# Performance work log

Hardware: AMD Instinct MI355X
Metric: run time of the kernel (lower is better)

Reference implementation:

```python
import jax, jax.numpy as jnp
import numpy as np

_MASK = -1.0e9
_EPS = 1e-8
B, N, E, D, L, NREL, TAU = 4, 2048, 32768, 128, 3, 1000, 0.1


def setup_inputs() -> dict:
    key = jax.random.key(0)
    ks = jax.random.split(key, 24)
    s = 0.05
    inp = {
        'edge_index': jax.random.randint(ks[0], (B, 2, E), 0, N, dtype=jnp.int32),
        'rels': jax.random.randint(ks[1], (B, E), 0, NREL, dtype=jnp.int32),
        'scores': jax.random.uniform(ks[2], (B, E), dtype=jnp.float32),
        'edge_conf_mask': jax.random.randint(ks[3], (B, E), 0, 2) > 0,
        'edge_mask': jax.random.randint(ks[4], (B, E), 0, 2) > 0,
        'mask': jnp.ones((B, N), dtype=bool),
        'r_query_embed': jax.random.normal(ks[5], (B, D), dtype=jnp.float32),
        'conf_embeds': jax.random.normal(ks[6], (B, E, D), dtype=jnp.float32),
        'rel_table': jax.random.normal(ks[7], (NREL, D), dtype=jnp.float32) * s,
        'beta_W': jax.random.normal(ks[8], (D, 1), dtype=jnp.float32) * s,
        'beta_b': jnp.zeros((1,), dtype=jnp.float32),
        'msg_W': jax.random.normal(ks[9], (L, 5 * D, D), dtype=jnp.float32) * s,
        'msg_b': jnp.zeros((L, D), dtype=jnp.float32),
        'upd_W': jax.random.normal(ks[10], (L, D, D), dtype=jnp.float32) * s,
        'upd_b': jnp.zeros((L, D), dtype=jnp.float32),
        'ln_g': jnp.ones((D,), dtype=jnp.float32),
        'ln_b': jnp.zeros((D,), dtype=jnp.float32),
        'att_W': jax.random.normal(ks[11], (L, 3 * D, 1), dtype=jnp.float32) * s,
        'att_b': jnp.zeros((L, 1), dtype=jnp.float32),
        'den_W1': jax.random.normal(ks[12], (3 * D, D), dtype=jnp.float32) * s,
        'den_b1': jnp.zeros((D,), dtype=jnp.float32),
        'den_W2': jax.random.normal(ks[13], (D, 1), dtype=jnp.float32) * s,
        'den_b2': jnp.zeros((1,), dtype=jnp.float32),
    }
    return inp


def _layer_norm(x, g, b, eps=1e-5):
    mu = jnp.mean(x, axis=-1, keepdims=True)
    var = jnp.var(x, axis=-1, keepdims=True)
    return (x - mu) * jax.lax.rsqrt(var + eps) * g + b


def reference(edge_index, rels, scores, edge_conf_mask, edge_mask, mask,
              r_query_embed, conf_embeds, rel_table, beta_W, beta_b,
              msg_W, msg_b, upd_W, upd_b, ln_g, ln_b, att_W, att_b,
              den_W1, den_b1, den_W2, den_b2):
    Bb, Nn = mask.shape
    Ee = edge_index.shape[2]
    d = rel_table.shape[1]
    bidx = jnp.arange(Bb)[:, None]                      # [B,1] batch index for scatter/gather
    src = edge_index[:, 0, :]                           # [B,E]
    tgt = edge_index[:, 1, :]                           # [B,E]

    h_init = jnp.zeros((Bb, Nn, d), dtype=rel_table.dtype).at[:, 0, :].set(1.0)
    h = h_init
    h_r = rel_table[rels]                               # [B,E,D]
    rq = jnp.broadcast_to(r_query_embed[:, None, :], (Bb, Ee, d))
    em = edge_mask.astype(h.dtype)[..., None]           # [B,E,1]

    # edge denoiser gate
    gate_in = jnp.concatenate([h_r, rq, conf_embeds], axis=-1)
    den = jax.nn.sigmoid(jax.nn.relu(gate_in @ den_W1 + den_b1) @ den_W2 + den_b2) * em

    beta = jax.nn.sigmoid((h_r + rq) @ beta_W + beta_b)             # [B,E,1]
    gate_known = jax.nn.sigmoid((scores[..., None] - beta) / TAU)
    gate = jnp.where(edge_conf_mask[..., None], gate_known, 0.5)

    outs = []
    for k in range(msg_W.shape[0]):
        h_src = h[bidx, src]                            # [B,E,D] gather
        h_init_src = h_init[bidx, src]
        msg_in = jnp.concatenate([h_src * h_r, h_src, h_init_src, h_r, conf_embeds], axis=-1)
        raw_msg = jax.nn.relu(msg_in @ msg_W[k] + msg_b[k])         # [B,E,D]

        att_in = jnp.concatenate([raw_msg, h_r, rq], axis=-1)
        att = jax.nn.leaky_relu((att_in @ att_W[k] + att_b[k])[..., 0], 0.01)
        att = jnp.where(edge_mask, att, _MASK)

        # scatter-softmax over edges sharing a target node
        mx = jnp.full((Bb, Nn), _MASK, dtype=att.dtype).at[bidx, tgt].max(att)
        ex = jnp.exp(att - mx[bidx, tgt])
        sm = jnp.zeros((Bb, Nn), dtype=att.dtype).at[bidx, tgt].add(ex)
        alpha = ex / (sm[bidx, tgt] + _EPS)             # [B,E]

        wmsg = gate * alpha[..., None] * raw_msg * em * den
        aggr = jnp.zeros_like(h).at[bidx, tgt].add(wmsg)
        h = _layer_norm(h + aggr @ upd_W[k] + upd_b[k], ln_g, ln_b)
        outs.append(h[:, 0, :])
    return jnp.stack(outs, axis=1)                      # [B,L,D]
```

## Files before the change

### kernel.cpp

```cpp
#include <hip/hip_runtime.h>
#include <stdint.h>
#include <math.h>

#define BB 4
#define NNODE 2048
#define NE 32768
#define DDIM 128
#define NL 3
#define NRELS 1000
#define MASKV -1000000000.0f

typedef unsigned short ushort_t;
typedef __attribute__((ext_vector_type(8))) short bfrag;
typedef __attribute__((ext_vector_type(4))) float f4;

__device__ __forceinline__ float sigf(float x){ return 1.0f/(1.0f+expf(-x)); }

__device__ __forceinline__ float bf2f(ushort_t u){
  union { unsigned int i; float f; } v; v.i = ((unsigned int)u) << 16; return v.f;
}
__device__ __forceinline__ ushort_t f2bf(float x){
  union { float f; unsigned int u; } v; v.f = x;
  unsigned int r = (v.u + 0x7FFFu + ((v.u >> 16) & 1u)) >> 16;
  return (ushort_t)r;
}
__device__ __forceinline__ float bflo(unsigned u){
  union{unsigned i;float f;}v; v.i=u<<16; return v.f;
}
__device__ __forceinline__ float bfhi(unsigned u){
  union{unsigned i;float f;}v; v.i=u&0xFFFF0000u; return v.f;
}
__device__ __forceinline__ unsigned pmul_bf(unsigned a, unsigned b){
  return (unsigned)f2bf(bflo(a)*bflo(b)) | ((unsigned)f2bf(bfhi(a)*bfhi(b))<<16);
}
__device__ __forceinline__ unsigned packbf(float a, float b){
  return (unsigned)f2bf(a) | ((unsigned)f2bf(b)<<16);
}

__global__ void probe_mask_kernel(const void* cm_raw, int* flag){
  int t = threadIdx.x;
  const int* ip = (const int*)cm_raw;
  unsigned v = (unsigned)ip[t];
  bool i32ok = (v <= 1u);
  bool f32ok = (v == 0u) || (v == 0x3F800000u);
  unsigned long long bi = __ballot(i32ok);
  unsigned long long bf_ = __ballot(f32ok);
  if (t == 0){
    int f;
    if (bi == ~0ULL) f = 0;
    else if (bf_ == ~0ULL) f = 1;
    else f = 2;
    *flag = f;
  }
}

__global__ void prep_kernel(const void* cm_raw, const void* em_raw, const int* __restrict__ flag,
    uint8_t* __restrict__ cm, uint8_t* __restrict__ em, int* __restrict__ deg,
    const float* __restrict__ relt, ushort_t* __restrict__ relt_bf,
    const float* __restrict__ rq, ushort_t* __restrict__ rq_bf,
    int* __restrict__ src_c, int* __restrict__ rel_c, int* __restrict__ ge_c,
    float* __restrict__ h, ushort_t* __restrict__ h_bf)
{
  int gid = blockIdx.x*256 + threadIdx.x;
  if (gid < BB*NE){
    int f = *flag; uint8_t c, e;
    if (f == 0){ c = ((const int*)cm_raw)[gid]!=0;   e = ((const int*)em_raw)[gid]!=0; }
    else if (f == 1){ c = ((const float*)cm_raw)[gid]!=0.0f; e = ((const float*)em_raw)[gid]!=0.0f; }
    else { c = ((const uint8_t*)cm_raw)[gid]!=0; e = ((const uint8_t*)em_raw)[gid]!=0; }
    cm[gid]=c; em[gid]=e;
    src_c[gid]=0; rel_c[gid]=0; ge_c[gid]=0;
  }
  if (gid < BB*NNODE) deg[gid]=0;
  if (gid < NRELS*DDIM/4){
    float4 v = *(const float4*)&relt[gid*4];
    ushort4 o; o.x=f2bf(v.x); o.y=f2bf(v.y); o.z=f2bf(v.z); o.w=f2bf(v.w);
    *(ushort4*)&relt_bf[gid*4] = o;
  }
  if (gid < BB*DDIM/4){
    float4 v = *(const float4*)&rq[gid*4];
    ushort4 o; o.x=f2bf(v.x); o.y=f2bf(v.y); o.z=f2bf(v.z); o.w=f2bf(v.w);
    *(ushort4*)&rq_bf[gid*4] = o;
  }
  {
    int base = gid*4;
    int nd = base & (NNODE*DDIM - 1);
    bool one = (nd < DDIM);
    float4 hv = one ? (float4){1.f,1.f,1.f,1.f} : (float4){0.f,0.f,0.f,0.f};
    ushort4 hb = one ? (ushort4){0x3F80,0x3F80,0x3F80,0x3F80} : (ushort4){0,0,0,0};
    *(float4*)&h[base] = hv;
    *(ushort4*)&h_bf[base] = hb;
  }
}

__global__ void csr_hist_kernel(const int* __restrict__ edge_index,
                                const uint8_t* __restrict__ em, int* __restrict__ deg){
  int gid = blockIdx.x*256 + threadIdx.x;
  if (!em[gid]) return;
  int b = gid >> 15, e = gid & (NE-1);
  int tgt = edge_index[(b<<16) + NE + e];
  atomicAdd(&deg[(b<<11) + tgt], 1);
}
__global__ void csr_scan_kernel(const int* __restrict__ deg,
                                int* __restrict__ base, int* __restrict__ cursor){
  __shared__ int part[256];
  int t = threadIdx.x;
  int loc[32]; int s = 0;
  #pragma unroll
  for (int i=0;i<32;++i){ loc[i] = deg[t*32+i]; s += loc[i]; }
  part[t] = s; __syncthreads();
  for (int off=1; off<256; off<<=1){
    int v = (t >= off) ? part[t-off] : 0;
    __syncthreads();
    part[t] += v;
    __syncthreads();
  }
  int ex = (t==0) ? 0 : part[t-1];
  #pragma unroll
  for (int i=0;i<32;++i){ base[t*32+i] = ex; cursor[t*32+i] = ex; ex += loc[i]; }
  if (t == 255) base[256*32] = ex;
}
__global__ void csr_scatter_kernel(const int* __restrict__ edge_index,
                                   const int* __restrict__ rels,
                                   const uint8_t* __restrict__ em,
                                   int* __restrict__ cursor,
                                   int* __restrict__ src_c, int* __restrict__ rel_c,
                                   int* __restrict__ ge_c){
  int gid = blockIdx.x*256 + threadIdx.x;
  if (!em[gid]) return;
  int b = gid >> 15, e = gid & (NE-1);
  int tgt = edge_index[(b<<16) + NE + e];
  int src = edge_index[(b<<16) + e];
  int pos = atomicAdd(&cursor[(b<<11) + tgt], 1);
  src_c[pos] = (b<<11) | src;
  rel_c[pos] = rels[gid];
  ge_c[pos]  = gid;
}

__global__ void precomp_tables_kernel(
    const float* __restrict__ relt, const float* __restrict__ rq,
    const float* __restrict__ attW, const float* __restrict__ betaW,
    float* __restrict__ att_rel, float* __restrict__ att_rq,
    float* __restrict__ beta_rel, float* __restrict__ beta_rq)
{
  int wid = (blockIdx.x*256 + threadIdx.x) >> 6;
  int lane = threadIdx.x & 63;
  if (wid >= 3*NRELS + 3*BB + NRELS + BB) return;
  const float* vec; const float* w; float* dst; int di;
  if (wid < 3*NRELS){
    int k = wid/NRELS, rl = wid%NRELS;
    vec = relt + rl*DDIM; w = attW + k*384 + 128; dst = att_rel; di = wid;
  } else if (wid < 3*NRELS + 3*BB){
    int idx = wid - 3*NRELS; int k = idx/BB, b = idx%BB;
    vec = rq + b*DDIM; w = attW + k*384 + 256; dst = att_rq; di = idx;
  } else if (wid < 3*NRELS + 3*BB + NRELS){
    int rl = wid - (3*NRELS + 3*BB);
    vec = relt + rl*DDIM; w = betaW; dst = beta_rel; di = rl;
  } else {
    int b = wid - (3*NRELS + 3*BB + NRELS);
    vec = rq + b*DDIM; w = betaW; dst = beta_rq; di = b;
  }
  float s = vec[lane]*w[lane] + vec[lane+64]*w[lane+64];
  #pragma unroll
  for (int off=32; off; off>>=1) s += __shfl_xor(s, off, 64);
  if (lane == 0) dst[di] = s;
}

__global__ void vtables_kernel(const float* __restrict__ relt, const float* __restrict__ rq,
    const float* __restrict__ msgW, const float* __restrict__ msgb,
    const float* __restrict__ denW1, const float* __restrict__ denb1,
    float* __restrict__ relmsg, float* __restrict__ relhh0,
    float* __restrict__ denrel, float* __restrict__ denrq,
    float* __restrict__ initvec, float* __restrict__ src0vec)
{
  int wv = (blockIdx.x*256 + threadIdx.x) >> 6;
  int lane = threadIdx.x & 63;
  if (wv >= 5008) return;
  const float* A = nullptr; const float* W; int K = 128; float* out; const float* bias = nullptr;
  if (wv < 3000){ int k=wv/1000, rl=wv%1000;
    A=relt+rl*128; W=msgW+(size_t)k*81920+49152; out=relmsg+(size_t)wv*128; bias=msgb+k*128; }
  else if (wv < 4000){ int rl=wv-3000;
    A=relt+rl*128; W=msgW; out=relhh0+(size_t)rl*128; }
  else if (wv < 5000){ int rl=wv-4000;
    A=relt+rl*128; W=denW1; out=denrel+(size_t)rl*128; }
  else if (wv < 5004){ int b=wv-5000;
    A=rq+b*128; W=denW1+16384; out=denrq+b*128; bias=denb1; }
  else if (wv < 5007){ int k=wv-5004;
    W=msgW+(size_t)k*81920+32768; out=initvec+k*128; }
  else { W=msgW+16384; K=256; out=src0vec; }
  float a0=0.f, a1=0.f;
  for (int kk=0; kk<K; ++kk){
    float av = A ? A[kk] : 1.0f;
    a0 = fmaf(av, W[kk*128+lane],    a0);
    a1 = fmaf(av, W[kk*128+lane+64], a1);
  }
  if (bias){ a0 += bias[lane]; a1 += bias[lane+64]; }
  out[lane]=a0; out[lane+64]=a1;
}

__global__ void build_wimg_kernel(const float* __restrict__ msgW,
                                  const float* __restrict__ denW1,
                                  ushort_t* __restrict__ img_msg,
                                  ushort_t* __restrict__ img_den){
  int e = blockIdx.x*256 + threadIdx.x;
  if (e >= 14*8192) return;
  int img_id = e >> 13;
  int ei = e & 8191;
  int j = ei >> 6;
  int kk = (((ei & 63) << 1) ^ ((j & 7) << 4)) >> 1;
  if (img_id < 12){
    int k = img_id >> 2, c = img_id & 3;
    int rowbase = (c < 2) ? c*64 : 512 + (c-2)*64;
    img_msg[(size_t)img_id*8192 + ei] = f2bf(msgW[(size_t)k*81920 + (rowbase+kk)*128 + j]);
  } else {
    int c = img_id - 12;
    int rowbase = 256 + c*64;
    img_den[(size_t)c*8192 + ei] = f2bf(denW1[(size_t)(rowbase+kk)*128 + j]);
  }
}

__global__ __launch_bounds__(256,2) void coef_mfma_kernel(
    const int* __restrict__ nact_p,
    const int* __restrict__ rel_c, const int* __restrict__ ge_c,
    const float* __restrict__ conf, const ushort_t* __restrict__ img_den,
    const float* __restrict__ denrel, const float* __restrict__ denrq,
    const float* __restrict__ denW2, const float* __restrict__ denb2,
    const float* __restrict__ scores, const uint8_t* __restrict__ cm,
    const float* __restrict__ beta_rel, const float* __restrict__ beta_rq,
    const float* __restrict__ betab,
    float* __restrict__ coef_c)
{
  __shared__ char lds[32768];
  __shared__ int rel_s[128], ge_s[128];
  __shared__ float w2_s[128];

  const int blk = blockIdx.x;
  const int ci0 = blk << 7;
  const int nact = *nact_p;
  if (ci0 >= nact) return;
  const int t = threadIdx.x;
  if (t < 128){ rel_s[t]=rel_c[ci0+t]; ge_s[t]=ge_c[ci0+t]; w2_s[t]=denW2[t]; }

  const int lane=t&63, wid=t>>6;
  const int wr=wid>>1, wc=wid&1;
  const int rbase=wr<<6, cbase=wc<<6;
  const int lr=lane&15, lk=lane>>4;
  const int swz=(lane&7)<<4;
  const int g=t&7, row0=t>>3;
  const int aswz=(g<<4)^((row0&7)<<4);

  f4 acc[4][4];
  #pragma unroll
  for (int m=0;m<4;++m)
    #pragma unroll
    for (int n=0;n<4;++n) acc[m][n]=(f4){0.f,0.f,0.f,0.f};

  const uint4* imgp = (const uint4*)img_den;
  float4 pf0[4], pf1[4];
  uint4 pb[4];
  __syncthreads();

  auto issueA = [&](int ch){
    const int d0=(ch&1)<<6;
    #pragma unroll
    for (int i=0;i<4;++i){
      int row=row0+(i<<5);
      const float* cp = conf + (((size_t)ge_s[row])<<7) + d0 + (g<<3);
      pf0[i]=*(const float4*)cp; pf1[i]=*(const float4*)(cp+4);
    }
    #pragma unroll
    for (int i=0;i<4;++i) pb[i]=imgp[ch*1024+(i<<8)+t];
  };

  issueA(0);
  #pragma unroll
  for (int ch=0; ch<2; ++ch){
    #pragma unroll
    for (int i=0;i<4;++i){
      int row=row0+(i<<5);
      uint4 val;
      val.x=packbf(pf0[i].x,pf0[i].y); val.y=packbf(pf0[i].z,pf0[i].w);
      val.z=packbf(pf1[i].x,pf1[i].y); val.w=packbf(pf1[i].z,pf1[i].w);
      *(uint4*)(lds + row*128 + aswz) = val;
    }
    *(uint4*)(lds+16384+(t<<4))        = pb[0];
    *(uint4*)(lds+16384+(t<<4)+4096)   = pb[1];
    *(uint4*)(lds+16384+(t<<4)+8192)   = pb[2];
    *(uint4*)(lds+16384+(t<<4)+12288)  = pb[3];
    __syncthreads();
    if (ch < 1) issueA(ch+1);
    #pragma unroll
    for (int s=0;s<2;++s){
      bfrag af[4], bfr[4];
      #pragma unroll
      for (int m=0;m<4;++m)
        af[m] = *(const bfrag*)(lds + (rbase+(m<<4)+lr)*128 + (((s<<6)+(lk<<4)) ^ swz));
      #pragma unroll
      for (int n=0;n<4;++n)
        bfr[n] = *(const bfrag*)(lds + 16384 + (cbase+(n<<4)+lr)*128 + (((s<<6)+(lk<<4)) ^ swz));
      #pragma unroll
      for (int m=0;m<4;++m)
        #pragma unroll
        for (int n=0;n<4;++n)
          acc[m][n] = __builtin_amdgcn_mfma_f32_16x16x32_bf16(af[m], bfr[n], acc[m][n], 0,0,0);
    }
    __syncthreads();
  }

  #pragma unroll
  for (int m=0;m<4;++m)
    #pragma unroll
    for (int n=0;n<4;++n)
      #pragma unroll
      for (int q=0;q<4;++q){
        int row=rbase+(m<<4)+(lk<<2)+q;
        int col=cbase+(n<<4)+lr;
        *(ushort_t*)(lds+(row<<8)+((col<<1)^((row&7)<<4))) = f2bf(acc[m][n][q]);
      }
  __syncthreads();

  #pragma unroll
  for (int i=0;i<8;++i){
    int u=t+(i<<8), row=u>>4, gg=u&15, c0=gg<<3;
    uint4 v = *(const uint4*)(lds+(row<<8)+((gg<<4)^((row&7)<<4)));
    float vv[8] = {bflo(v.x),bfhi(v.x),bflo(v.y),bfhi(v.y),
                   bflo(v.z),bfhi(v.z),bflo(v.w),bfhi(v.w)};
    int rel=rel_s[row], ge=ge_s[row], b=ge>>15;
    const float* dr = denrel + ((size_t)rel<<7) + c0;
    const float* dq = denrq + (b<<7) + c0;
    float part=0.f;
    #pragma unroll
    for (int j=0;j<8;++j){
      float m = fmaxf(vv[j] + dr[j] + dq[j], 0.f);
      part = fmaf(m, w2_s[c0+j], part);
    }
    #pragma unroll
    for (int off=1; off<16; off<<=1) part += __shfl_xor(part, off, 16);
    if (gg == 0){
      float den = sigf(part + denb2[0]);
      float beta = sigf(beta_rel[rel] + beta_rq[b] + betab[0]);
      float gt = cm[ge] ? sigf((scores[ge]-beta)*10.0f) : 0.5f;
      coef_c[ci0+row] = gt * den;
    }
  }
}

template<bool L0>
__global__ __launch_bounds__(256,2) void msg_mfma_kernel(
    const int* __restrict__ nact_p,
    const int* __restrict__ src_c, const int* __restrict__ rel_c,
    const int* __restrict__ ge_c,
    const ushort_t* __restrict__ relt_bf, const float* __restrict__ conf,
    const ushort_t* __restrict__ h_bf, const float* __restrict__ H1,
    const ushort_t* __restrict__ img_msg,
    const float* __restrict__ relmsg, const float* __restrict__ relhh0,
    const float* __restrict__ src0vec, const float* __restrict__ initvec,
    const float* __restrict__ attW, const float* __restrict__ attb,
    const float* __restrict__ att_rel, const float* __restrict__ att_rq,
    ushort_t* __restrict__ raw_c, float* __restrict__ att_c, int layer)
{
  constexpr int NCH = L0 ? 2 : 4;
  __shared__ char lds[32768];
  __shared__ int src_s[128], rel_s[128], ge_s[128];
  __shared__ float attw_s[128];

  const int blk = blockIdx.x;
  const int ci0 = blk << 7;
  const int nact = *nact_p;
  if (ci0 >= nact) return;
  const int t = threadIdx.x;
  if (t < 128){
    src_s[t]=src_c[ci0+t]; rel_s[t]=rel_c[ci0+t]; ge_s[t]=ge_c[ci0+t];
    attw_s[t]=attW[layer*384+t];
  }

  const int lane=t&63, wid=t>>6;
  const int wr=wid>>1, wc=wid&1;
  const int rbase=wr<<6, cbase=wc<<6;
  const int lr=lane&15, lk=lane>>4;
  const int swz=(lane&7)<<4;
  const int g=t&7, row0=t>>3;
  const int aswz=(g<<4)^((row0&7)<<4);

  f4 acc[4][4];
  #pragma unroll
  for (int m=0;m<4;++m)
    #pragma unroll
    for (int n=0;n<4;++n) acc[m][n]=(f4){0.f,0.f,0.f,0.f};

  const uint4* imgp = (const uint4*)(img_msg + (size_t)layer*4*8192);
  uint4 pa[4], pr[4], pb[4];
  float4 pf0[4], pf1[4];
  __syncthreads();

  auto issueA = [&](int ch){
    const int d0=(ch&1)<<6;
    const bool cf = L0 || (ch>=2);
    #pragma unroll
    for (int i=0;i<4;++i){
      int row=row0+(i<<5);
      if (cf){
        const float* cp = conf + (((size_t)ge_s[row])<<7) + d0 + (g<<3);
        pf0[i]=*(const float4*)cp; pf1[i]=*(const float4*)(cp+4);
      } else {
        pa[i]=*(const uint4*)&h_bf[(((size_t)src_s[row])<<7)+d0+(g<<3)];
        pr[i]=*(const uint4*)&relt_bf[(((size_t)rel_s[row])<<7)+d0+(g<<3)];
      }
    }
    int ic = L0 ? ch+2 : ch;
    #pragma unroll
    for (int i=0;i<4;++i) pb[i]=imgp[ic*1024+(i<<8)+t];
  };

  issueA(0);
  #pragma unroll
  for (int ch=0; ch<NCH; ++ch){
    const bool cf = L0 || (ch>=2);
    #pragma unroll
    for (int i=0;i<4;++i){
      int row=row0+(i<<5);
      uint4 val;
      if (cf){
        val.x=packbf(pf0[i].x,pf0[i].y); val.y=packbf(pf0[i].z,pf0[i].w);
        val.z=packbf(pf1[i].x,pf1[i].y); val.w=packbf(pf1[i].z,pf1[i].w);
      } else {
        val.x=pmul_bf(pa[i].x,pr[i].x); val.y=pmul_bf(pa[i].y,pr[i].y);
        val.z=pmul_bf(pa[i].z,pr[i].z); val.w=pmul_bf(pa[i].w,pr[i].w);
      }
      *(uint4*)(lds + row*128 + aswz) = val;
    }
    *(uint4*)(lds+16384+(t<<4))        = pb[0];
    *(uint4*)(lds+16384+(t<<4)+4096)   = pb[1];
    *(uint4*)(lds+16384+(t<<4)+8192)   = pb[2];
    *(uint4*)(lds+16384+(t<<4)+12288)  = pb[3];
    __syncthreads();
    if (ch < NCH-1) issueA(ch+1);
    #pragma unroll
    for (int s=0;s<2;++s){
      bfrag af[4], bfr[4];
      #pragma unroll
      for (int m=0;m<4;++m)
        af[m] = *(const bfrag*)(lds + (rbase+(m<<4)+lr)*128 + (((s<<6)+(lk<<4)) ^ swz));
      #pragma unroll
      for (int n=0;n<4;++n)
        bfr[n] = *(const bfrag*)(lds + 16384 + (cbase+(n<<4)+lr)*128 + (((s<<6)+(lk<<4)) ^ swz));
      #pragma unroll
      for (int m=0;m<4;++m)
        #pragma unroll
        for (int n=0;n<4;++n)
          acc[m][n] = __builtin_amdgcn_mfma_f32_16x16x32_bf16(af[m], bfr[n], acc[m][n], 0,0,0);
    }
    __syncthreads();
  }

  #pragma unroll
  for (int m=0;m<4;++m)
    #pragma unroll
    for (int n=0;n<4;++n)
      #pragma unroll
      for (int q=0;q<4;++q){
        int row=rbase+(m<<4)+(lk<<2)+q;
        int col=cbase+(n<<4)+lr;
        *(ushort_t*)(lds+(row<<8)+((col<<1)^((row&7)<<4))) = f2bf(acc[m][n][q]);
      }
  __syncthreads();

  #pragma unroll
  for (int i=0;i<8;++i){
    int u=t+(i<<8), row=u>>4, gg=u&15, c0=gg<<3;
    uint4 v = *(const uint4*)(lds+(row<<8)+((gg<<4)^((row&7)<<4)));
    float vv[8] = {bflo(v.x),bfhi(v.x),bflo(v.y),bfhi(v.y),
                   bflo(v.z),bfhi(v.z),bflo(v.w),bfhi(v.w)};
    int rel=rel_s[row], sc=src_s[row], ge=ge_s[row], b=ge>>15;
    const float* rm = relmsg + (((size_t)(layer*1000+rel))<<7) + c0;
    float bias[8];
    #pragma unroll
    for (int j=0;j<8;++j) bias[j] = rm[j];
    if (!L0){
      const float* hp = H1 + (((size_t)sc)<<7) + c0;
      #pragma unroll
      for (int j=0;j<8;++j) bias[j] += hp[j];
      if ((sc & (NNODE-1)) == 0){
        const float* iv = initvec + layer*128 + c0;
        #pragma unroll
        for (int j=0;j<8;++j) bias[j] += iv[j];
      }
    } else {
      if ((sc & (NNODE-1)) == 0){
        const float* rh = relhh0 + ((size_t)rel<<7) + c0;
        const float* sv = src0vec + c0;
        #pragma unroll
        for (int j=0;j<8;++j) bias[j] += rh[j] + sv[j];
      }
    }
    float part=0.f;
    unsigned o0,o1,o2,o3;
    {
      float m0=fmaxf(vv[0]+bias[0],0.f), m1=fmaxf(vv[1]+bias[1],0.f);
      float m2=fmaxf(vv[2]+bias[2],0.f), m3=fmaxf(vv[3]+bias[3],0.f);
      float m4=fmaxf(vv[4]+bias[4],0.f), m5=fmaxf(vv[5]+bias[5],0.f);
      float m6=fmaxf(vv[6]+bias[6],0.f), m7=fmaxf(vv[7]+bias[7],0.f);
      part = m0*attw_s[c0] + m1*attw_s[c0+1] + m2*attw_s[c0+2] + m3*attw_s[c0+3]
           + m4*attw_s[c0+4] + m5*attw_s[c0+5] + m6*attw_s[c0+6] + m7*attw_s[c0+7];
      o0=packbf(m0,m1); o1=packbf(m2,m3); o2=packbf(m4,m5); o3=packbf(m6,m7);
    }
    uint4 ov; ov.x=o0; ov.y=o1; ov.z=o2; ov.w=o3;
    *(uint4*)&raw_c[(((size_t)(ci0+row))<<7) + c0] = ov;
    #pragma unroll
    for (int off=1; off<16; off<<=1) part += __shfl_xor(part, off, 16);
    if (gg == 0){
      float a = part + att_rel[layer*NRELS+rel] + att_rq[layer*BB+b] + attb[layer];
      a = (a >= 0.f) ? a : 0.01f*a;
      att_c[ci0+row] = a;
    }
  }
}

#define FMA4(acc, a, bv) do { \
    acc.x = fmaf(a, bv.x, acc.x); \
    acc.y = fmaf(a, bv.y, acc.y); \
    acc.z = fmaf(a, bv.z, acc.z); \
    acc.w = fmaf(a, bv.w, acc.w); } while(0)

__global__ __launch_bounds__(256,2) void h1_gemm_kernel(
    const float* __restrict__ h, const float* __restrict__ msgW,
    float* __restrict__ H1, int layer)
{
  __shared__ float As[64*65];
  __shared__ float Bs[64*128];
  const int t = threadIdx.x, blk = blockIdx.x;
  const int n0 = blk << 6;
  const int c = t & 15, r = t >> 4;
  float4 acc0[4], acc1[4];
  #pragma unroll
  for (int i=0;i<4;++i){ acc0[i]=make_float4(0,0,0,0); acc1[i]=make_float4(0,0,0,0); }
  const float* wbase = msgW + (size_t)layer*81920 + 16384;

  for (int ch=0; ch<2; ++ch){
    __syncthreads();
    #pragma unroll
    for (int l=0;l<16;++l){
      int idx=(l<<8)+t, ei=idx>>6, kk=idx&63;
      As[ei*65+kk] = h[(size_t)(n0+ei)*DDIM + (ch<<6) + kk];
    }
    #pragma unroll
    for (int l=0;l<32;++l){
      int idx=(l<<8)+t, kk=idx>>7, j=idx&127;
      Bs[(kk<<7)+j] = wbase[((ch<<6)+kk)*DDIM + j];
    }
    __syncthreads();
    #pragma unroll 4
    for (int kk=0;kk<64;++kk){
      const float4 b0 = *(const float4*)&Bs[(kk<<7) + (c<<2)];
      const float4 b1 = *(const float4*)&Bs[(kk<<7) + 64 + (c<<2)];
      #pragma unroll
      for (int i=0;i<4;++i){
        const float a = As[((r<<2)+i)*65 + kk];
        FMA4(acc0[i], a, b0);
        FMA4(acc1[i], a, b1);
      }
    }
  }
  const int col0 = c << 2;
  #pragma unroll
  for (int i=0;i<4;++i){
    const int row = n0 + (r<<2) + i;
    *(float4*)&H1[(size_t)row*DDIM + col0]      = make_float4(acc0[i].x,acc0[i].y,acc0[i].z,acc0[i].w);
    *(float4*)&H1[(size_t)row*DDIM + 64 + col0] = make_float4(acc1[i].x,acc1[i].y,acc1[i].z,acc1[i].w);
  }
}

__global__ __launch_bounds__(128) void node_agg_kernel(
    const int* __restrict__ base,
    const float* __restrict__ att_c, const float* __restrict__ coef_c,
    const ushort_t* __restrict__ raw_c, float* __restrict__ aggr)
{
  const int n = blockIdx.x;
  const int t = threadIdx.x;
  const int b0 = base[n], b1 = base[n+1];
  const int deg = b1 - b0;
  if (deg == 0){ aggr[((size_t)n<<7)+t] = 0.f; return; }
  __shared__ float w_s[128];
  __shared__ float red[4];
  float mx = -3.0e38f;
  for (int j=t; j<deg; j+=128) mx = fmaxf(mx, att_c[b0+j]);
  #pragma unroll
  for (int o=1;o<64;o<<=1) mx = fmaxf(mx, __shfl_xor(mx, o, 64));
  if ((t&63)==0) red[t>>6] = mx;
  __syncthreads();
  mx = fmaxf(red[0], red[1]);
  float s = 0.f;
  for (int j=t; j<deg; j+=128) s += expf(att_c[b0+j]-mx);
  #pragma unroll
  for (int o=1;o<64;o<<=1) s += __shfl_xor(s, o, 64);
  if ((t&63)==0) red[2+(t>>6)] = s;
  __syncthreads();
  const float inv = 1.0f/((red[2]+red[3]) + 1e-8f);
  float accv = 0.f;
  for (int jb=0; jb<deg; jb+=128){
    int jj = jb + t;
    __syncthreads();
    if (jj < deg) w_s[t] = coef_c[b0+jj] * expf(att_c[b0+jj]-mx) * inv;
    __syncthreads();
    int lim = min(128, deg-jb);
    for (int j=0; j<lim; ++j)
      accv = fmaf(w_s[j], bf2f(raw_c[(((size_t)(b0+jb+j))<<7)+t]), accv);
  }
  aggr[((size_t)n<<7)+t] = accv;
}

__global__ __launch_bounds__(256,2) void update_kernel(
    const float* __restrict__ aggr, const float* __restrict__ updW,
    const float* __restrict__ updb,
    const float* __restrict__ lng, const float* __restrict__ lnb,
    float* __restrict__ h, ushort_t* __restrict__ h_bf,
    float* __restrict__ out, int layer)
{
  __shared__ float As[64*65];
  __shared__ float Bs[64*128];
  const int t = threadIdx.x, blk = blockIdx.x;
  const int n0 = blk << 6;
  const int c = t & 15, r = t >> 4;
  float4 acc0[4], acc1[4];
  #pragma unroll
  for (int i=0;i<4;++i){ acc0[i]=make_float4(0,0,0,0); acc1[i]=make_float4(0,0,0,0); }
  const float* wbase = updW + (size_t)layer*DDIM*DDIM;

  for (int ch=0; ch<2; ++ch){
    __syncthreads();
    #pragma unroll
    for (int l=0;l<16;++l){
      int idx=(l<<8)+t, ei=idx>>6, kk=idx&63;
      As[ei*65+kk] = aggr[(size_t)(n0+ei)*DDIM + (ch<<6) + kk];
    }
    #pragma unroll
    for (int l=0;l<32;++l){
      int idx=(l<<8)+t, kk=idx>>7, j=idx&127;
      Bs[(kk<<7)+j] = wbase[((ch<<6)+kk)*DDIM + j];
    }
    __syncthreads();
    #pragma unroll 4
    for (int kk=0;kk<64;++kk){
      const float4 b0 = *(const float4*)&Bs[(kk<<7) + (c<<2)];
      const float4 b1 = *(const float4*)&Bs[(kk<<7) + 64 + (c<<2)];
      #pragma unroll
      for (int i=0;i<4;++i){
        const float a = As[((r<<2)+i)*65 + kk];
        FMA4(acc0[i], a, b0);
        FMA4(acc1[i], a, b1);
      }
    }
  }

  const int col0 = c << 2;
  float ub0[4], ub1[4], g0[4], g1[4], lb0[4], lb1[4];
  #pragma unroll
  for (int q=0;q<4;++q){
    ub0[q] = updb[layer*DDIM + col0+q];  ub1[q] = updb[layer*DDIM + 64+col0+q];
    g0[q]  = lng[col0+q];                g1[q]  = lng[64+col0+q];
    lb0[q] = lnb[col0+q];                lb1[q] = lnb[64+col0+q];
  }

  #pragma unroll
  for (int i=0;i<4;++i){
    const int row = n0 + (r<<2) + i;
    float* hrow = h + (size_t)row*DDIM;
    float4 h0 = *(float4*)&hrow[col0];
    float4 h1 = *(float4*)&hrow[64+col0];
    float x0[4], x1[4];
    x0[0] = h0.x + acc0[i].x + ub0[0];
    x0[1] = h0.y + acc0[i].y + ub0[1];
    x0[2] = h0.z + acc0[i].z + ub0[2];
    x0[3] = h0.w + acc0[i].w + ub0[3];
    x1[0] = h1.x + acc1[i].x + ub1[0];
    x1[1] = h1.y + acc1[i].y + ub1[1];
    x1[2] = h1.z + acc1[i].z + ub1[2];
    x1[3] = h1.w + acc1[i].w + ub1[3];
    float s = 0.f, s2 = 0.f;
    #pragma unroll
    for (int q=0;q<4;++q){ s += x0[q]+x1[q]; s2 += x0[q]*x0[q] + x1[q]*x1[q]; }
    #pragma unroll
    for (int off=1; off<16; off<<=1){
      s  += __shfl_xor(s,  off, 16);
      s2 += __shfl_xor(s2, off, 16);
    }
    const float mu = s * (1.0f/128.0f);
    const float var = s2 * (1.0f/128.0f) - mu*mu;
    const float rstd = rsqrtf(var + 1e-5f);
    float4 y0, y1;
    y0.x = (x0[0]-mu)*rstd*g0[0] + lb0[0];
    y0.y = (x0[1]-mu)*rstd*g0[1] + lb0[1];
    y0.z = (x0[2]-mu)*rstd*g0[2] + lb0[2];
    y0.w = (x0[3]-mu)*rstd*g0[3] + lb0[3];
    y1.x = (x1[0]-mu)*rstd*g1[0] + lb1[0];
    y1.y = (x1[1]-mu)*rstd*g1[1] + lb1[1];
    y1.z = (x1[2]-mu)*rstd*g1[2] + lb1[2];
    y1.w = (x1[3]-mu)*rstd*g1[3] + lb1[3];
    *(float4*)&hrow[col0] = y0;
    *(float4*)&hrow[64+col0] = y1;
    ushort4 z0, z1;
    z0.x=f2bf(y0.x); z0.y=f2bf(y0.y); z0.z=f2bf(y0.z); z0.w=f2bf(y0.w);
    z1.x=f2bf(y1.x); z1.y=f2bf(y1.y); z1.z=f2bf(y1.z); z1.w=f2bf(y1.w);
    *(ushort4*)&h_bf[(size_t)row*DDIM + col0] = z0;
    *(ushort4*)&h_bf[(size_t)row*DDIM + 64 + col0] = z1;
    if ((row & (NNODE-1)) == 0){
      const int bb_ = row >> 11;
      float* op = out + (size_t)(bb_*NL + layer)*DDIM;
      *(float4*)&op[col0] = y0;
      *(float4*)&op[64+col0] = y1;
    }
  }
}

extern "C" void kernel_launch(void* const* d_in, const int* in_sizes, int n_in,
                              void* d_out, int out_size, void* d_ws, size_t ws_size,
                              hipStream_t stream) {
  const int*   edge_index = (const int*)d_in[0];
  const int*   rels       = (const int*)d_in[1];
  const float* scores     = (const float*)d_in[2];
  const void*  cm_raw     = d_in[3];
  const void*  em_raw     = d_in[4];
  const float* rq    = (const float*)d_in[6];
  const float* conf  = (const float*)d_in[7];
  const float* relt  = (const float*)d_in[8];
  const float* betaW = (const float*)d_in[9];
  const float* betab = (const float*)d_in[10];
  const float* msgW  = (const float*)d_in[11];
  const float* msgb  = (const float*)d_in[12];
  const float* updW  = (const float*)d_in[13];
  const float* updb  = (const float*)d_in[14];
  const float* lng   = (const float*)d_in[15];
  const float* lnb   = (const float*)d_in[16];
  const float* attW  = (const float*)d_in[17];
  const float* attb  = (const float*)d_in[18];
  const float* denW1 = (const float*)d_in[19];
  const float* denb1 = (const float*)d_in[20];
  const float* denW2 = (const float*)d_in[21];
  const float* denb2 = (const float*)d_in[22];
  float* out = (float*)d_out;
  char* ws = (char*)d_ws;

  size_t off = 0;
  float* h        = (float*)(ws + off); off += (size_t)BB*NNODE*DDIM*4;
  ushort_t* h_bf  = (ushort_t*)(ws + off); off += (size_t)BB*NNODE*DDIM*2;
  float* aggr     = (float*)(ws + off); off += (size_t)BB*NNODE*DDIM*4;
  float* H1       = (float*)(ws + off); off += (size_t)BB*NNODE*DDIM*4;
  ushort_t* raw_c = (ushort_t*)(ws + off); off += (size_t)BB*NE*DDIM*2;
  float* att_c    = (float*)(ws + off); off += (size_t)BB*NE*4;
  float* coef_c   = (float*)(ws + off); off += (size_t)BB*NE*4;
  int* src_c      = (int*)(ws + off); off += (size_t)BB*NE*4;
  int* rel_c      = (int*)(ws + off); off += (size_t)BB*NE*4;
  int* ge_c       = (int*)(ws + off); off += (size_t)BB*NE*4;
  int* deg        = (int*)(ws + off); off += (size_t)BB*NNODE*4;
  int* base       = (int*)(ws + off); off += (size_t)(BB*NNODE+16)*4;
  int* cursor     = (int*)(ws + off); off += (size_t)BB*NNODE*4;
  ushort_t* relt_bf = (ushort_t*)(ws + off); off += (size_t)NRELS*DDIM*2 + 64;
  ushort_t* rq_bf   = (ushort_t*)(ws + off); off += (size_t)BB*DDIM*2 + 64;
  ushort_t* img_msg = (ushort_t*)(ws + off); off += (size_t)12*8192*2;
  ushort_t* img_den = (ushort_t*)(ws + off); off += (size_t)2*8192*2;
  float* relmsg   = (float*)(ws + off); off += (size_t)3*NRELS*DDIM*4;
  float* relhh0   = (float*)(ws + off); off += (size_t)NRELS*DDIM*4;
  float* denrel   = (float*)(ws + off); off += (size_t)NRELS*DDIM*4;
  float* denrq    = (float*)(ws + off); off += (size_t)BB*DDIM*4;
  float* initvec  = (float*)(ws + off); off += 3*DDIM*4;
  float* src0vec  = (float*)(ws + off); off += DDIM*4;
  float* att_rel  = (float*)(ws + off); off += 3*NRELS*4 + 32;
  float* att_rq   = (float*)(ws + off); off += 64;
  float* beta_rel = (float*)(ws + off); off += NRELS*4 + 32;
  float* beta_rq  = (float*)(ws + off); off += 64;
  uint8_t* cm_dec = (uint8_t*)(ws + off); off += (size_t)BB*NE;
  uint8_t* em_dec = (uint8_t*)(ws + off); off += (size_t)BB*NE;
  int* flag       = (int*)(ws + off); off += 64;

  probe_mask_kernel<<<1, 64, 0, stream>>>(cm_raw, flag);
  prep_kernel<<<1024, 256, 0, stream>>>(cm_raw, em_raw, flag, cm_dec, em_dec, deg,
                                        relt, relt_bf, rq, rq_bf,
                                        src_c, rel_c, ge_c, h, h_bf);
  csr_hist_kernel<<<512, 256, 0, stream>>>(edge_index, em_dec, deg);
  csr_scan_kernel<<<1, 256, 0, stream>>>(deg, base, cursor);
  csr_scatter_kernel<<<512, 256, 0, stream>>>(edge_index, rels, em_dec, cursor,
                                              src_c, rel_c, ge_c);
  precomp_tables_kernel<<<1004, 256, 0, stream>>>(relt, rq, attW, betaW,
                                                  att_rel, att_rq, beta_rel, beta_rq);
  vtables_kernel<<<1252, 256, 0, stream>>>(relt, rq, msgW, msgb, denW1, denb1,
                                           relmsg, relhh0, denrel, denrq,
                                           initvec, src0vec);
  build_wimg_kernel<<<448, 256, 0, stream>>>(msgW, denW1, img_msg, img_den);
  coef_mfma_kernel<<<1024, 256, 0, stream>>>(base + BB*NNODE, rel_c, ge_c, conf, img_den,
                                             denrel, denrq, denW2, denb2,
                                             scores, cm_dec, beta_rel, beta_rq, betab,
                                             coef_c);
  for (int k = 0; k < NL; ++k){
    if (k == 0){
      msg_mfma_kernel<true><<<1024, 256, 0, stream>>>(base + BB*NNODE, src_c, rel_c, ge_c,
          relt_bf, conf, h_bf, H1, img_msg, relmsg, relhh0, src0vec, initvec,
          attW, attb, att_rel, att_rq, raw_c, att_c, k);
    } else {
      h1_gemm_kernel<<<128, 256, 0, stream>>>(h, msgW, H1, k);
      msg_mfma_kernel<false><<<1024, 256, 0, stream>>>(base + BB*NNODE, src_c, rel_c, ge_c,
          relt_bf, conf, h_bf, H1, img_msg, relmsg, relhh0, src0vec, initvec,
          attW, attb, att_rel, att_rq, raw_c, att_c, k);
    }
    node_agg_kernel<<<BB*NNODE, 128, 0, stream>>>(base, att_c, coef_c, raw_c, aggr);
    update_kernel<<<128, 256, 0, stream>>>(aggr, updW, updb, lng, lnb, h, h_bf, out, k);
  }
}
```

Baseline: 413.3 us.

## Compute relation tables with bf16 MFMA GEMM and fold small kernels together

The scalar vtables kernel is replaced. It used one wave per output row with serial FMA loops over 5000 relation-table rows. In its place, a bf16 MFMA tile GEMM (table_gemm_kernel) runs over swizzled bf16 weight images that build_wimg_kernel now also produces. The few remaining small vector products move into precomp_tables_kernel with an unrolled loop. The mask-format probe is folded into prep_kernel through a per-block ballot in shared memory. Together these cut two launches and the slow scalar table build, at the cost of bf16 rounding in tables that were fp32 before.

```diff
diff --git a/kernel.cpp b/kernel.cpp
--- a/kernel.cpp
+++ b/kernel.cpp
@@ -37,33 +37,27 @@
   return (unsigned)f2bf(a) | ((unsigned)f2bf(b)<<16);
 }
 
-__global__ void probe_mask_kernel(const void* cm_raw, int* flag){
-  int t = threadIdx.x;
-  const int* ip = (const int*)cm_raw;
-  unsigned v = (unsigned)ip[t];
-  bool i32ok = (v <= 1u);
-  bool f32ok = (v == 0u) || (v == 0x3F800000u);
-  unsigned long long bi = __ballot(i32ok);
-  unsigned long long bf_ = __ballot(f32ok);
-  if (t == 0){
-    int f;
-    if (bi == ~0ULL) f = 0;
-    else if (bf_ == ~0ULL) f = 1;
-    else f = 2;
-    *flag = f;
-  }
-}
-
-__global__ void prep_kernel(const void* cm_raw, const void* em_raw, const int* __restrict__ flag,
+__global__ void prep_kernel(const void* cm_raw, const void* em_raw,
     uint8_t* __restrict__ cm, uint8_t* __restrict__ em, int* __restrict__ deg,
     const float* __restrict__ relt, ushort_t* __restrict__ relt_bf,
     const float* __restrict__ rq, ushort_t* __restrict__ rq_bf,
     int* __restrict__ src_c, int* __restrict__ rel_c, int* __restrict__ ge_c,
     float* __restrict__ h, ushort_t* __restrict__ h_bf)
 {
+  __shared__ int flag_s;
+  if (threadIdx.x < 64){
+    unsigned v = ((const unsigned*)cm_raw)[threadIdx.x];
+    bool i32ok = (v <= 1u);
+    bool f32ok = (v == 0u) || (v == 0x3F800000u);
+    unsigned long long bi = __ballot(i32ok);
+    unsigned long long bf_ = __ballot(f32ok);
+    if (threadIdx.x == 0) flag_s = (bi==~0ULL) ? 0 : ((bf_==~0ULL) ? 1 : 2);
+  }
+  __syncthreads();
+  const int f = flag_s;
   int gid = blockIdx.x*256 + threadIdx.x;
   if (gid < BB*NE){
-    int f = *flag; uint8_t c, e;
+    uint8_t c, e;
     if (f == 0){ c = ((const int*)cm_raw)[gid]!=0;   e = ((const int*)em_raw)[gid]!=0; }
     else if (f == 1){ c = ((const float*)cm_raw)[gid]!=0.0f; e = ((const float*)em_raw)[gid]!=0.0f; }
     else { c = ((const uint8_t*)cm_raw)[gid]!=0; e = ((const uint8_t*)em_raw)[gid]!=0; }
@@ -139,15 +133,42 @@
 __global__ void precomp_tables_kernel(
     const float* __restrict__ relt, const float* __restrict__ rq,
     const float* __restrict__ attW, const float* __restrict__ betaW,
+    const float* __restrict__ msgW, const float* __restrict__ denW1,
+    const float* __restrict__ denb1,
     float* __restrict__ att_rel, float* __restrict__ att_rq,
-    float* __restrict__ beta_rel, float* __restrict__ beta_rq)
+    float* __restrict__ beta_rel, float* __restrict__ beta_rq,
+    float* __restrict__ denrq, float* __restrict__ initvec,
+    float* __restrict__ src0vec)
 {
   int wid = (blockIdx.x*256 + threadIdx.x) >> 6;
   int lane = threadIdx.x & 63;
-  if (wid >= 3*NRELS + 3*BB + NRELS + BB) return;
+  if (wid >= 4024) return;
+  if (wid >= 4016){
+    int widx = wid - 4016;
+    const float* A = nullptr; const float* W; int K = 128;
+    float* outp; const float* bias = nullptr;
+    if (widx < 4){ A = rq + widx*128; W = denW1 + 16384; outp = denrq + widx*128; bias = denb1; }
+    else if (widx < 7){ int k=widx-4; W = msgW + (size_t)k*81920 + 32768; outp = initvec + k*128; }
+    else { W = msgW + 16384; K = 256; outp = src0vec; }
+    float a0=0.f, a1=0.f;
+    for (int kk=0; kk<K; kk+=8){
+      float av[8], w0[8], w1[8];
+      #pragma unroll
+      for (int u=0;u<8;++u){
+        av[u] = A ? A[kk+u] : 1.0f;
+        w0[u] = W[(size_t)(kk+u)*128 + lane];
+        w1[u] = W[(size_t)(kk+u)*128 + lane + 64];
+      }
+      #pragma unroll
+      for (int u=0;u<8;++u){ a0 = fmaf(av[u], w0[u], a0); a1 = fmaf(av[u], w1[u], a1); }
+    }
+    if (bias){ a0 += bias[lane]; a1 += bias[lane+64]; }
+    outp[lane] = a0; outp[lane+64] = a1;
+    return;
+  }
   const float* vec; const float* w; float* dst; int di;
   if (wid < 3*NRELS){
-    int k = wid/NRELS, rl = wid%NRELS;
+    int k = wid/1000, rl = wid%1000;
     vec = relt + rl*DDIM; w = attW + k*384 + 128; dst = att_rel; di = wid;
   } else if (wid < 3*NRELS + 3*BB){
     int idx = wid - 3*NRELS; int k = idx/BB, b = idx%BB;
@@ -165,57 +186,130 @@
   if (lane == 0) dst[di] = s;
 }
 
-__global__ void vtables_kernel(const float* __restrict__ relt, const float* __restrict__ rq,
-    const float* __restrict__ msgW, const float* __restrict__ msgb,
-    const float* __restrict__ denW1, const float* __restrict__ denb1,
-    float* __restrict__ relmsg, float* __restrict__ relhh0,
-    float* __restrict__ denrel, float* __restrict__ denrq,
-    float* __restrict__ initvec, float* __restrict__ src0vec)
-{
-  int wv = (blockIdx.x*256 + threadIdx.x) >> 6;
-  int lane = threadIdx.x & 63;
-  if (wv >= 5008) return;
-  const float* A = nullptr; const float* W; int K = 128; float* out; const float* bias = nullptr;
-  if (wv < 3000){ int k=wv/1000, rl=wv%1000;
-    A=relt+rl*128; W=msgW+(size_t)k*81920+49152; out=relmsg+(size_t)wv*128; bias=msgb+k*128; }
-  else if (wv < 4000){ int rl=wv-3000;
-    A=relt+rl*128; W=msgW; out=relhh0+(size_t)rl*128; }
-  else if (wv < 5000){ int rl=wv-4000;
-    A=relt+rl*128; W=denW1; out=denrel+(size_t)rl*128; }
-  else if (wv < 5004){ int b=wv-5000;
-    A=rq+b*128; W=denW1+16384; out=denrq+b*128; bias=denb1; }
-  else if (wv < 5007){ int k=wv-5004;
-    W=msgW+(size_t)k*81920+32768; out=initvec+k*128; }
-  else { W=msgW+16384; K=256; out=src0vec; }
-  float a0=0.f, a1=0.f;
-  for (int kk=0; kk<K; ++kk){
-    float av = A ? A[kk] : 1.0f;
-    a0 = fmaf(av, W[kk*128+lane],    a0);
-    a1 = fmaf(av, W[kk*128+lane+64], a1);
-  }
-  if (bias){ a0 += bias[lane]; a1 += bias[lane+64]; }
-  out[lane]=a0; out[lane+64]=a1;
-}
-
 __global__ void build_wimg_kernel(const float* __restrict__ msgW,
                                   const float* __restrict__ denW1,
                                   ushort_t* __restrict__ img_msg,
-                                  ushort_t* __restrict__ img_den){
+                                  ushort_t* __restrict__ img_den,
+                                  ushort_t* __restrict__ img_tab){
   int e = blockIdx.x*256 + threadIdx.x;
-  if (e >= 14*8192) return;
+  if (e >= 22*8192) return;
   int img_id = e >> 13;
   int ei = e & 8191;
   int j = ei >> 6;
   int kk = (((ei & 63) << 1) ^ ((j & 7) << 4)) >> 1;
+  float v;
+  ushort_t* dst;
   if (img_id < 12){
     int k = img_id >> 2, c = img_id & 3;
     int rowbase = (c < 2) ? c*64 : 512 + (c-2)*64;
-    img_msg[(size_t)img_id*8192 + ei] = f2bf(msgW[(size_t)k*81920 + (rowbase+kk)*128 + j]);
+    v = msgW[(size_t)k*81920 + (rowbase+kk)*128 + j];
+    dst = img_msg + (size_t)img_id*8192;
+  } else if (img_id < 14){
+    int c = img_id - 12;
+    v = denW1[(size_t)(256 + c*64 + kk)*128 + j];
+    dst = img_den + (size_t)c*8192;
+  } else if (img_id < 20){
+    int idx = img_id - 14, k = idx >> 1, c = idx & 1;
+    v = msgW[(size_t)k*81920 + (384 + c*64 + kk)*128 + j];
+    dst = img_tab + (size_t)idx*8192;
   } else {
-    int c = img_id - 12;
-    int rowbase = 256 + c*64;
-    img_den[(size_t)c*8192 + ei] = f2bf(denW1[(size_t)(rowbase+kk)*128 + j]);
-  }
+    int c = img_id - 20;
+    v = denW1[(size_t)(c*64 + kk)*128 + j];
+    dst = img_tab + (size_t)(6+c)*8192;
+  }
+  dst[ei] = f2bf(v);
+}
+
+__global__ __launch_bounds__(256,2) void table_gemm_kernel(
+    const ushort_t* __restrict__ relt_bf, const ushort_t* __restrict__ img_msg,
+    const ushort_t* __restrict__ img_tab, const float* __restrict__ msgb,
+    float* __restrict__ relmsg, float* __restrict__ relhh0,
+    float* __restrict__ denrel)
+{
+  __shared__ char lds[32768];
+  __shared__ float bias_s[128];
+  const int blk = blockIdx.x;
+  const int job = blk % 5;
+  const int ri0 = (blk/5) << 7;
+  const int t = threadIdx.x;
+  const uint4* imgb;
+  float* outp;
+  if (job < 3){ imgb = (const uint4*)(img_tab + (size_t)(2*job)*8192); outp = relmsg + (size_t)job*NRELS*DDIM; }
+  else if (job == 3){ imgb = (const uint4*)img_msg; outp = relhh0; }
+  else { imgb = (const uint4*)(img_tab + (size_t)6*8192); outp = denrel; }
+  if (t < 128) bias_s[t] = (job < 3) ? msgb[job*128 + t] : 0.f;
+
+  const int lane=t&63, wid=t>>6;
+  const int wr=wid>>1, wc=wid&1;
+  const int rbase=wr<<6, cbase=wc<<6;
+  const int lr=lane&15, lk=lane>>4;
+  const int swz=(lane&7)<<4;
+  const int g=t&7, row0=t>>3;
+  const int aswz=(g<<4)^((row0&7)<<4);
+
+  f4 acc[4][4];
+  #pragma unroll
+  for (int m=0;m<4;++m)
+    #pragma unroll
+    for (int n=0;n<4;++n) acc[m][n]=(f4){0.f,0.f,0.f,0.f};
+
+  uint4 pa[4], pb[4];
+  auto issueA = [&](int ch){
+    #pragma unroll
+    for (int i=0;i<4;++i){
+      int rr = ri0 + row0 + (i<<5);
+      rr = (rr < NRELS) ? rr : (NRELS-1);
+      pa[i] = *(const uint4*)&relt_bf[(size_t)rr*128 + (ch<<6) + (g<<3)];
+    }
+    #pragma unroll
+    for (int i=0;i<4;++i) pb[i] = imgb[ch*1024 + (i<<8) + t];
+  };
+
+  __syncthreads();
+  issueA(0);
+  #pragma unroll
+  for (int ch=0; ch<2; ++ch){
+    #pragma unroll
+    for (int i=0;i<4;++i){
+      int row = row0 + (i<<5);
+      *(uint4*)(lds + row*128 + aswz) = pa[i];
+    }
+    *(uint4*)(lds+16384+(t<<4))        = pb[0];
+    *(uint4*)(lds+16384+(t<<4)+4096)   = pb[1];
+    *(uint4*)(lds+16384+(t<<4)+8192)   = pb[2];
+    *(uint4*)(lds+16384+(t<<4)+12288)  = pb[3];
+    __syncthreads();
+    if (ch < 1) issueA(ch+1);
+    #pragma unroll
+    for (int s=0;s<2;++s){
+      bfrag af[4], bfr[4];
+      #pragma unroll
+      for (int m=0;m<4;++m)
+        af[m] = *(const bfrag*)(lds + (rbase+(m<<4)+lr)*128 + (((s<<6)+(lk<<4)) ^ swz));
+      #pragma unroll
+      for (int n=0;n<4;++n)
+        bfr[n] = *(const bfrag*)(lds + 16384 + (cbase+(n<<4)+lr)*128 + (((s<<6)+(lk<<4)) ^ swz));
+      #pragma unroll
+      for (int m=0;m<4;++m)
+        #pragma unroll
+        for (int n=0;n<4;++n)
+          acc[m][n] = __builtin_amdgcn_mfma_f32_16x16x32_bf16(af[m], bfr[n], acc[m][n], 0,0,0);
+    }
+    __syncthreads();
+  }
+
+  #pragma unroll
+  for (int m=0;m<4;++m)
+    #pragma unroll
+    for (int n=0;n<4;++n){
+      int col = cbase + (n<<4) + lr;
+      float bv = bias_s[col];
+      #pragma unroll
+      for (int q=0;q<4;++q){
+        int gr = ri0 + rbase + (m<<4) + (lk<<2) + q;
+        if (gr < NRELS) outp[(size_t)gr*128 + col] = acc[m][n][q] + bv;
+      }
+    }
 }
 
 __global__ __launch_bounds__(256,2) void coef_mfma_kernel(
@@ -471,7 +565,7 @@
     float vv[8] = {bflo(v.x),bfhi(v.x),bflo(v.y),bfhi(v.y),
                    bflo(v.z),bfhi(v.z),bflo(v.w),bfhi(v.w)};
     int rel=rel_s[row], sc=src_s[row], ge=ge_s[row], b=ge>>15;
-    const float* rm = relmsg + (((size_t)(layer*1000+rel))<<7) + c0;
+    const float* rm = relmsg + (((size_t)(layer*NRELS+rel))<<7) + c0;
     float bias[8];
     #pragma unroll
     for (int j=0;j<8;++j) bias[j] = rm[j];
@@ -757,6 +851,7 @@
   ushort_t* rq_bf   = (ushort_t*)(ws + off); off += (size_t)BB*DDIM*2 + 64;
   ushort_t* img_msg = (ushort_t*)(ws + off); off += (size_t)12*8192*2;
   ushort_t* img_den = (ushort_t*)(ws + off); off += (size_t)2*8192*2;
+  ushort_t* img_tab = (ushort_t*)(ws + off); off += (size_t)8*8192*2;
   float* relmsg   = (float*)(ws + off); off += (size_t)3*NRELS*DDIM*4;
   float* relhh0   = (float*)(ws + off); off += (size_t)NRELS*DDIM*4;
   float* denrel   = (float*)(ws + off); off += (size_t)NRELS*DDIM*4;
@@ -769,22 +864,21 @@
   float* beta_rq  = (float*)(ws + off); off += 64;
   uint8_t* cm_dec = (uint8_t*)(ws + off); off += (size_t)BB*NE;
   uint8_t* em_dec = (uint8_t*)(ws + off); off += (size_t)BB*NE;
-  int* flag       = (int*)(ws + off); off += 64;
-
-  probe_mask_kernel<<<1, 64, 0, stream>>>(cm_raw, flag);
-  prep_kernel<<<1024, 256, 0, stream>>>(cm_raw, em_raw, flag, cm_dec, em_dec, deg,
+
+  prep_kernel<<<1024, 256, 0, stream>>>(cm_raw, em_raw, cm_dec, em_dec, deg,
                                         relt, relt_bf, rq, rq_bf,
                                         src_c, rel_c, ge_c, h, h_bf);
   csr_hist_kernel<<<512, 256, 0, stream>>>(edge_index, em_dec, deg);
   csr_scan_kernel<<<1, 256, 0, stream>>>(deg, base, cursor);
   csr_scatter_kernel<<<512, 256, 0, stream>>>(edge_index, rels, em_dec, cursor,
                                               src_c, rel_c, ge_c);
-  precomp_tables_kernel<<<1004, 256, 0, stream>>>(relt, rq, attW, betaW,
-                                                  att_rel, att_rq, beta_rel, beta_rq);
-  vtables_kernel<<<1252, 256, 0, stream>>>(relt, rq, msgW, msgb, denW1, denb1,
-                                           relmsg, relhh0, denrel, denrq,
-                                           initvec, src0vec);
-  build_wimg_kernel<<<448, 256, 0, stream>>>(msgW, denW1, img_msg, img_den);
+  precomp_tables_kernel<<<1006, 256, 0, stream>>>(relt, rq, attW, betaW,
+                                                  msgW, denW1, denb1,
+                                                  att_rel, att_rq, beta_rel, beta_rq,
+                                                  denrq, initvec, src0vec);
+  build_wimg_kernel<<<704, 256, 0, stream>>>(msgW, denW1, img_msg, img_den, img_tab);
+  table_gemm_kernel<<<40, 256, 0, stream>>>(relt_bf, img_msg, img_tab, msgb,
+                                            relmsg, relhh0, denrel);
   coef_mfma_kernel<<<1024, 256, 0, stream>>>(base + BB*NNODE, rel_c, ge_c, conf, img_den,
                                              denrel, denrq, denW2, denb2,
                                              scores, cm_dec, beta_rel, beta_rq, betab,
```

Measured after the change: 382.7 us. 7.4% less time.
